# Optimization experiments

Measured on AMD Instinct MI355X. Metric: run time of the kernel, lower is better.

The kernel has to match this reference:

```python
import jax, jax.numpy as jnp
import numpy as np

N = 8192      # num nodes = feature dim (A is NxN adjacency used as features)
H = 1024      # bottleneck dim
E = 8192      # num edges
PENALTY = 10.0  # scalar buffer from __init__


def setup_inputs() -> dict:
    key = jax.random.key(0)
    ks = jax.random.split(key, 7)
    return {
        "A": jax.random.normal(ks[0], (N, N), dtype=jnp.float32),
        "W1": jax.random.normal(ks[1], (H, N), dtype=jnp.float32) * 0.02,
        "b1": jax.random.normal(ks[2], (H,), dtype=jnp.float32) * 0.02,
        "W2": jax.random.normal(ks[3], (N, H), dtype=jnp.float32) * 0.02,
        "b2": jax.random.normal(ks[4], (N,), dtype=jnp.float32) * 0.02,
        "edges": jax.random.randint(ks[5], (E, 2), 0, N, dtype=jnp.int32),
        "labels": jax.random.randint(ks[6], (E,), 0, 2, dtype=jnp.int32),
    }


def reference(A, W1, b1, W2, b2, edges, labels):
    ni = edges[:, 0]
    nj = edges[:, 1]
    Xi = A[ni]  # [E, N]
    Xj = A[nj]  # [E, N]
    lab = labels.astype(A.dtype)

    layers = [(W1, b1), (W2, b2)]
    Hi, Hj = Xi, Xj
    loss_1 = jnp.zeros((), A.dtype)
    loss_r_per_edge = jnp.zeros((), A.dtype)
    for (W, b) in layers:
        Hi = jax.nn.sigmoid(Hi @ W.T + b)
        Hj = jax.nn.sigmoid(Hj @ W.T + b)
        # per-edge L2 norm of activation diff at this layer, weighted by label
        loss_1 = loss_1 + jnp.sum(jnp.linalg.norm(Hi - Hj, axis=1) * lab)
        # original code appends weight-row-norm sum + bias norm once per (edge, layer)
        loss_r_per_edge = loss_r_per_edge + jnp.sum(jnp.linalg.norm(W, axis=1)) + jnp.linalg.norm(b)
    loss_r = loss_r_per_edge * jnp.asarray(E, A.dtype)

    # reconstruction loss; penalty scales the diff when label >= 1 (scalar => factors out of norm)
    factor = jnp.where(lab >= 1.0, jnp.asarray(PENALTY, A.dtype), jnp.asarray(1.0, A.dtype))
    loss_2 = jnp.sum(factor * (jnp.linalg.norm(Xi - Hi, axis=1) + jnp.linalg.norm(Xj - Hj, axis=1)))

    return loss_1 + loss_2 + loss_r
```

## Files before the change

### kernel.cpp

```cpp
#include <hip/hip_runtime.h>
#include <hip/hip_bf16.h>
#include <stdint.h>

#define N_DIM 8192
#define H_DIM 1024
#define E_DIM 8192
#define PENALTY_F 10.0f
#define WSCALE 16.0f
#define INV_WSCALE 0.0625f

typedef unsigned short u16;
typedef unsigned char u8;
typedef unsigned int u32;
typedef __attribute__((ext_vector_type(4))) float f32x4;
typedef __attribute__((ext_vector_type(2))) float f32x2;
typedef __attribute__((ext_vector_type(4))) int i32x4;
typedef __attribute__((ext_vector_type(8))) int i32x8;

__device__ __forceinline__ u32 pack4_fp8(float a, float b, float c, float d) {
  u32 p = __builtin_amdgcn_cvt_pk_fp8_f32(a, b, 0, false);
  p = __builtin_amdgcn_cvt_pk_fp8_f32(c, d, p, true);
  return p;
}
__device__ __forceinline__ f32x2 unpk_lo(u32 v) {
  return __builtin_amdgcn_cvt_pk_f32_fp8(v, false);
}
__device__ __forceinline__ f32x2 unpk_hi(u32 v) {
  return __builtin_amdgcn_cvt_pk_f32_fp8(v, true);
}

#define GLD16(ldsptr, gptr)                                                     \
  __builtin_amdgcn_global_load_lds(                                             \
      (__attribute__((address_space(1))) void*)(gptr),                          \
      (__attribute__((address_space(3))) void*)(ldsptr), 16, 0, 0)

#define PSLOT(part) (&(part)[(blockIdx.x & 63) * 16])

__device__ __forceinline__ float wave_red(float v) {
  for (int o = 32; o; o >>= 1) v += __shfl_down(v, o, 64);
  return v;
}

__device__ __forceinline__ float block_reduce1(float v) {
  __shared__ float buf[4];
  v = wave_red(v);
  int lane = threadIdx.x & 63, w = threadIdx.x >> 6;
  if (lane == 0) buf[w] = v;
  __syncthreads();
  float r = 0.f;
  if (threadIdx.x == 0) r = buf[0] + buf[1] + buf[2] + buf[3];
  return r;
}

__global__ void convert_f32_fp8(const float* __restrict__ in,
                                u8* __restrict__ out, int n4, float scale) {
  const int stride = gridDim.x * blockDim.x;
  for (int i = blockIdx.x * blockDim.x + threadIdx.x; i < n4; i += stride) {
    float4 v = ((const float4*)in)[i];
    ((u32*)out)[i] =
        pack4_fp8(v.x * scale, v.y * scale, v.z * scale, v.w * scale);
  }
}

__global__ void prep_w(const float* __restrict__ W1,
                       const float* __restrict__ W2,
                       const float* __restrict__ b1,
                       const float* __restrict__ b2, u8* __restrict__ W1_8,
                       u8* __restrict__ W2_8, float* __restrict__ part) {
  const int blk = blockIdx.x;
  float* slotp = PSLOT(part);
  if (blk < H_DIM) {
    const float4* row = (const float4*)(W1 + (size_t)blk * N_DIM);
    u32* orow = (u32*)(W1_8 + (size_t)blk * N_DIM);
    float s = 0.f;
#pragma unroll
    for (int t = 0; t < 8; ++t) {
      int i = threadIdx.x + t * 256;
      float4 v = row[i];
      s += v.x * v.x + v.y * v.y + v.z * v.z + v.w * v.w;
      orow[i] = pack4_fp8(v.x * WSCALE, v.y * WSCALE, v.z * WSCALE,
                          v.w * WSCALE);
    }
    s = block_reduce1(s);
    if (threadIdx.x == 0) atomicAdd(slotp, sqrtf(s) * (float)E_DIM);
  } else if (blk < H_DIM + N_DIM / 4) {
    __shared__ float buf[4];
    const int wave = threadIdx.x >> 6, lane = threadIdx.x & 63;
    const int r = (blk - H_DIM) * 4 + wave;
    const float4* row = (const float4*)(W2 + (size_t)r * H_DIM);
    u32* orow = (u32*)(W2_8 + (size_t)r * H_DIM);
    float s = 0.f;
#pragma unroll
    for (int t = 0; t < 4; ++t) {
      int i = lane + t * 64;
      float4 v = row[i];
      s += v.x * v.x + v.y * v.y + v.z * v.z + v.w * v.w;
      orow[i] = pack4_fp8(v.x * WSCALE, v.y * WSCALE, v.z * WSCALE,
                          v.w * WSCALE);
    }
    s = wave_red(s);
    if (lane == 0) buf[wave] = sqrtf(s);
    __syncthreads();
    if (threadIdx.x == 0)
      atomicAdd(slotp, (buf[0] + buf[1] + buf[2] + buf[3]) * (float)E_DIM);
  } else if (blk == H_DIM + N_DIM / 4) {
    const float4* row = (const float4*)b1;
    float4 v = row[threadIdx.x];
    float s = v.x * v.x + v.y * v.y + v.z * v.z + v.w * v.w;
    s = block_reduce1(s);
    if (threadIdx.x == 0) atomicAdd(slotp, sqrtf(s) * (float)E_DIM);
  } else {
    const float4* row = (const float4*)b2;
    float s = 0.f;
#pragma unroll
    for (int t = 0; t < 8; ++t) {
      float4 v = row[threadIdx.x + t * 256];
      s += v.x * v.x + v.y * v.y + v.z * v.z + v.w * v.w;
    }
    s = block_reduce1(s);
    if (threadIdx.x == 0) atomicAdd(slotp, sqrtf(s) * (float)E_DIM);
  }
}

#define BM 128
#define BN 128
#define BKB 128

__global__ __launch_bounds__(256) void gemm_fp8_sigmoid(
    const u8* __restrict__ Ag,
    const u8* __restrict__ Bg,
    const float* __restrict__ bias,
    u8* __restrict__ Cg,
    float invScale, int K, int Nd) {
  __shared__ __align__(16) u8 Xs[BM * BKB];
  __shared__ __align__(16) u8 Ws[BN * BKB];

  const int nwg = gridDim.x * gridDim.y;
  const int id = blockIdx.y * gridDim.x + blockIdx.x;
  const int wg = (id & 7) * (nwg >> 3) + (id >> 3);
  const int bx = wg % gridDim.x;
  const int by = wg / gridDim.x;

  const int tid = threadIdx.x;
  const int wave = tid >> 6, lane = tid & 63;
  const int wr = wave >> 1, wc = wave & 1;
  const size_t rowBase = (size_t)by * BM;
  const size_t colBase = (size_t)bx * BN;

  f32x4 acc[4][4] = {};

  const int i8 = lane >> 3;
  const int c8 = lane & 7;
  const int sw = c8 ^ i8;

  const int quad = lane >> 4;
  const int m15 = lane & 15;

  for (int k0 = 0; k0 < K; k0 += BKB) {
#pragma unroll
    for (int j = 0; j < 4; ++j) {
      const int r0 = (wave * 4 + j) * 8;
      const u8* gx = Ag + (rowBase + r0 + i8) * (size_t)K + (k0 + sw * 16);
      GLD16(&Xs[r0 * BKB], gx);
      const u8* gw = Bg + (colBase + r0 + i8) * (size_t)K + (k0 + sw * 16);
      GLD16(&Ws[r0 * BKB], gw);
    }
    __syncthreads();

    i32x8 af[4], bfr[4];
#pragma unroll
    for (int t = 0; t < 4; ++t) {
      const int m = wr * 64 + t * 16 + m15;
      i32x4 alo = *(const i32x4*)&Xs[m * BKB + ((2 * quad) ^ (m & 7)) * 16];
      i32x4 ahi = *(const i32x4*)&Xs[m * BKB + ((2 * quad + 1) ^ (m & 7)) * 16];
      af[t] = __builtin_shufflevector(alo, ahi, 0, 1, 2, 3, 4, 5, 6, 7);
      const int n = wc * 64 + t * 16 + m15;
      i32x4 blo = *(const i32x4*)&Ws[n * BKB + ((2 * quad) ^ (n & 7)) * 16];
      i32x4 bhi = *(const i32x4*)&Ws[n * BKB + ((2 * quad + 1) ^ (n & 7)) * 16];
      bfr[t] = __builtin_shufflevector(blo, bhi, 0, 1, 2, 3, 4, 5, 6, 7);
    }
#pragma unroll
    for (int mt = 0; mt < 4; ++mt)
#pragma unroll
      for (int nt = 0; nt < 4; ++nt)
        acc[mt][nt] = __builtin_amdgcn_mfma_scale_f32_16x16x128_f8f6f4(
            bfr[nt], af[mt], acc[mt][nt], 0, 0,
            0, 0x7F7F7F7F, 0, 0x7F7F7F7F);
    __syncthreads();
  }

  f32x4 bv4[4];
#pragma unroll
  for (int nt = 0; nt < 4; ++nt)
    bv4[nt] = *(const f32x4*)&bias[colBase + wc * 64 + nt * 16 + quad * 4];
#pragma unroll
  for (int mt = 0; mt < 4; ++mt) {
    const size_t grow = rowBase + wr * 64 + mt * 16 + m15;
    u32* crow = (u32*)(Cg + grow * (size_t)Nd + colBase + wc * 64);
#pragma unroll
    for (int nt = 0; nt < 4; ++nt) {
      float v[4];
#pragma unroll
      for (int i = 0; i < 4; ++i) {
        float x = acc[mt][nt][i] * invScale + bv4[nt][i];
        v[i] = WSCALE / (1.0f + __expf(-x));
      }
      crow[nt * 4 + quad] = pack4_fp8(v[0], v[1], v[2], v[3]);
    }
  }
}

#define BM2 256
#define BN2 256

__global__ __launch_bounds__(512, 2) void gemm2_fp8_sigmoid(
    const u8* __restrict__ Ag,
    const u8* __restrict__ Bg,
    const float* __restrict__ bias,
    u8* __restrict__ Cg,
    const u8* __restrict__ A8,
    float* __restrict__ nd2,
    float invScale, int K, int Nd) {
  __shared__ __align__(16) u8 Xs[2][BM2 * BKB];
  __shared__ __align__(16) u8 Ws[2][BN2 * BKB];

  const int tid = threadIdx.x;
  const int wave = tid >> 6, lane = tid & 63;
  const int wr = wave >> 2;
  const int wc = wave & 3;
  const size_t rowBase = (size_t)blockIdx.y * BM2;
  const size_t colBase = (size_t)blockIdx.x * BN2;

  f32x4 acc[8][4] = {};

  const int i8 = lane >> 3;
  const int c8 = lane & 7;
  const int sw = c8 ^ i8;
  const int quad = lane >> 4;
  const int m15 = lane & 15;

  const int T = K / BKB;

  auto STAGE = [&](int kt, int b) {
    const size_t kOff = (size_t)kt * BKB + sw * 16;
#pragma unroll
    for (int j = 0; j < 4; ++j) {
      const int r0 = (wave * 4 + j) * 8;
      GLD16(&Xs[b][r0 * BKB], Ag + (rowBase + r0 + i8) * (size_t)K + kOff);
      GLD16(&Ws[b][r0 * BKB], Bg + (colBase + r0 + i8) * (size_t)K + kOff);
    }
  };

  STAGE(0, 0);
  __syncthreads();

  for (int t = 0; t < T; ++t) {
    const int cur = t & 1;
    if (t + 1 < T) STAGE(t + 1, cur ^ 1);

    const u8* Xb = Xs[cur];
    const u8* Wb = Ws[cur];

    i32x8 bfr[4];
#pragma unroll
    for (int nt = 0; nt < 4; ++nt) {
      const int n = wc * 64 + nt * 16 + m15;
      i32x4 blo = *(const i32x4*)&Wb[n * BKB + ((2 * quad) ^ (n & 7)) * 16];
      i32x4 bhi = *(const i32x4*)&Wb[n * BKB + ((2 * quad + 1) ^ (n & 7)) * 16];
      bfr[nt] = __builtin_shufflevector(blo, bhi, 0, 1, 2, 3, 4, 5, 6, 7);
    }
    __builtin_amdgcn_s_setprio(1);
#pragma unroll
    for (int mt = 0; mt < 8; ++mt) {
      const int m = wr * 128 + mt * 16 + m15;
      i32x4 alo = *(const i32x4*)&Xb[m * BKB + ((2 * quad) ^ (m & 7)) * 16];
      i32x4 ahi = *(const i32x4*)&Xb[m * BKB + ((2 * quad + 1) ^ (m & 7)) * 16];
      i32x8 af = __builtin_shufflevector(alo, ahi, 0, 1, 2, 3, 4, 5, 6, 7);
#pragma unroll
      for (int nt = 0; nt < 4; ++nt)
        acc[mt][nt] = __builtin_amdgcn_mfma_scale_f32_16x16x128_f8f6f4(
            bfr[nt], af, acc[mt][nt], 0, 0,
            0, 0x7F7F7F7F, 0, 0x7F7F7F7F);
    }
    __builtin_amdgcn_s_setprio(0);
    __syncthreads();
  }

  float* ndbuf = (float*)&Xs[0][0];
  if (tid < 256) ndbuf[tid] = 0.f;
  __syncthreads();

  f32x4 bv4[4];
#pragma unroll
  for (int nt = 0; nt < 4; ++nt)
    bv4[nt] = *(const f32x4*)&bias[colBase + wc * 64 + nt * 16 + quad * 4];
#pragma unroll
  for (int mt = 0; mt < 8; ++mt) {
    const int rowLocal = wr * 128 + mt * 16 + m15;
    const size_t grow = rowBase + rowLocal;
    u32* crow = (u32*)(Cg + grow * (size_t)Nd + colBase + wc * 64);
    const u32* arow = (const u32*)(A8 + grow * (size_t)Nd + colBase + wc * 64);
    float nds = 0.f;
#pragma unroll
    for (int nt = 0; nt < 4; ++nt) {
      float v[4];
#pragma unroll
      for (int i = 0; i < 4; ++i) {
        float x = acc[mt][nt][i] * invScale + bv4[nt][i];
        v[i] = WSCALE / (1.0f + __expf(-x));
      }
      const u32 packed = pack4_fp8(v[0], v[1], v[2], v[3]);
      crow[nt * 4 + quad] = packed;
      f32x2 hlo = unpk_lo(packed), hhi = unpk_hi(packed);
      const u32 xa = arow[nt * 4 + quad];
      f32x2 xlo = unpk_lo(xa), xhi = unpk_hi(xa);
      float d;
      d = WSCALE * xlo.x - hlo.x; nds += d * d;
      d = WSCALE * xlo.y - hlo.y; nds += d * d;
      d = WSCALE * xhi.x - hhi.x; nds += d * d;
      d = WSCALE * xhi.y - hhi.y; nds += d * d;
    }
    atomicAdd(&ndbuf[rowLocal], nds);
  }
  __syncthreads();
  if (tid < 256) atomicAdd(&nd2[rowBase + tid], ndbuf[tid]);
}

__global__ void edge_loss_h(const u8* __restrict__ H1,
                            const int* __restrict__ edges,
                            const int* __restrict__ labels,
                            float* __restrict__ part) {
  __shared__ float buf[4];
  const int wave = threadIdx.x >> 6, lane = threadIdx.x & 63;
  const int e = blockIdx.x * 4 + wave;
  float r = 0.f;
  if (labels[e] != 0) {
    const int ni = edges[e * 2], nj = edges[e * 2 + 1];
    const i32x4 a = ((const i32x4*)(H1 + (size_t)ni * H_DIM))[lane];
    const i32x4 b = ((const i32x4*)(H1 + (size_t)nj * H_DIM))[lane];
    float s = 0.f;
#pragma unroll
    for (int j = 0; j < 4; ++j) {
      f32x2 al = unpk_lo((u32)a[j]), ah = unpk_hi((u32)a[j]);
      f32x2 bl = unpk_lo((u32)b[j]), bh = unpk_hi((u32)b[j]);
      float d0 = al.x - bl.x, d1 = al.y - bl.y;
      float d2 = ah.x - bh.x, d3 = ah.y - bh.y;
      s += d0 * d0 + d1 * d1 + d2 * d2 + d3 * d3;
    }
    s = wave_red(s);
    r = sqrtf(s) * INV_WSCALE;
  }
  if (lane == 0) buf[wave] = r;
  __syncthreads();
  if (threadIdx.x == 0)
    atomicAdd(PSLOT(part), buf[0] + buf[1] + buf[2] + buf[3]);
}

__global__ void edge_loss_final(const u8* __restrict__ H2,
                                const float* __restrict__ nd2,
                                const int* __restrict__ edges,
                                const int* __restrict__ labels,
                                float* __restrict__ part) {
  __shared__ float buf[4];
  const int wave = threadIdx.x >> 6, lane = threadIdx.x & 63;
  const int e = blockIdx.x * 4 + wave;
  const int ni = edges[e * 2], nj = edges[e * 2 + 1];
  const i32x4* hi = (const i32x4*)(H2 + (size_t)ni * N_DIM);
  const i32x4* hj = (const i32x4*)(H2 + (size_t)nj * N_DIM);
  float s12 = 0.f;
#pragma unroll 2
  for (int t = 0; t < 8; ++t) {
    const int idx = lane + t * 64;
    i32x4 a = hi[idx], b = hj[idx];
#pragma unroll
    for (int j = 0; j < 4; ++j) {
      f32x2 al = unpk_lo((u32)a[j]), ah = unpk_hi((u32)a[j]);
      f32x2 bl = unpk_lo((u32)b[j]), bh = unpk_hi((u32)b[j]);
      float d;
      d = al.x - bl.x; s12 += d * d;
      d = al.y - bl.y; s12 += d * d;
      d = ah.x - bh.x; s12 += d * d;
      d = ah.y - bh.y; s12 += d * d;
    }
  }
  s12 = wave_red(s12);
  if (lane == 0) {
    float lab = (labels[e] != 0) ? 1.f : 0.f;
    float fac = (labels[e] != 0) ? PENALTY_F : 1.f;
    buf[wave] = (lab * sqrtf(s12) + fac * (sqrtf(nd2[ni]) + sqrtf(nd2[nj]))) *
                INV_WSCALE;
  }
  __syncthreads();
  if (threadIdx.x == 0)
    atomicAdd(PSLOT(part), buf[0] + buf[1] + buf[2] + buf[3]);
}

__global__ void finalize_sum(const float* __restrict__ part,
                             float* __restrict__ out) {
  float v = part[threadIdx.x * 16];
  v = wave_red(v);
  if (threadIdx.x == 0) atomicAdd(out, v);
}

extern "C" void kernel_launch(void* const* d_in, const int* in_sizes, int n_in,
                              void* d_out, int out_size, void* d_ws,
                              size_t ws_size, hipStream_t stream) {
  const float* A = (const float*)d_in[0];
  const float* W1 = (const float*)d_in[1];
  const float* b1 = (const float*)d_in[2];
  const float* W2 = (const float*)d_in[3];
  const float* b2 = (const float*)d_in[4];
  const int* edges = (const int*)d_in[5];
  const int* labels = (const int*)d_in[6];
  float* out = (float*)d_out;

  char* ws = (char*)d_ws;
  u8* A8   = (u8*)(ws);
  u8* H1_8 = (u8*)(ws + 67108864ull);
  u8* H2_8 = (u8*)(ws + 75497472ull);
  u8* W1_8 = (u8*)(ws + 142606336ull);
  u8* W2_8 = (u8*)(ws + 150994944ull);
  float* nd2  = (float*)(ws + 159383552ull);
  float* part = (float*)(ws + 159416320ull);

  hipMemsetAsync(out, 0, sizeof(float), stream);
  hipMemsetAsync(nd2, 0, N_DIM * sizeof(float) + 64 * 16 * sizeof(float),
                 stream);

  convert_f32_fp8<<<2048, 256, 0, stream>>>(A, A8, N_DIM * N_DIM / 4, 1.0f);

  prep_w<<<H_DIM + N_DIM / 4 + 2, 256, 0, stream>>>(W1, W2, b1, b2, W1_8,
                                                    W2_8, part);

  gemm_fp8_sigmoid<<<dim3(H_DIM / BN, N_DIM / BM), 256, 0, stream>>>(
      A8, W1_8, b1, H1_8, INV_WSCALE, N_DIM, H_DIM);
  edge_loss_h<<<E_DIM / 4, 256, 0, stream>>>(H1_8, edges, labels, part);

  gemm2_fp8_sigmoid<<<dim3(N_DIM / BN2, N_DIM / BM2), 512, 0, stream>>>(
      H1_8, W2_8, b2, H2_8, A8, nd2, INV_WSCALE * INV_WSCALE, H_DIM, N_DIM);
  edge_loss_final<<<E_DIM / 4, 256, 0, stream>>>(H2_8, nd2, edges, labels,
                                                 part);

  finalize_sum<<<1, 64, 0, stream>>>(part, out);
}
```

Before: 653.8 us.

## Fuse prep and edge kernels, drop memsets, use per-block partial slots

The A fp8 conversion, the weight prep and the nd2 zeroing are merged into one launch, which removes both memsets. The two edge-loss kernels become one that reads H2 rows only for labelled edges, since unlabelled edges contribute nothing from that term. Global atomics into 64 hashed slots are replaced by deterministic per-block partial writes that a 256-thread finalize sums. gemm2 also pre-reduces the row-norm partials with shuffles before its LDS atomics. Together these cut launch overhead, atomic contention and edge-phase memory traffic, at the cost of a larger finalize reduction.

```diff
diff --git a/kernel.cpp b/kernel.cpp
--- a/kernel.cpp
+++ b/kernel.cpp
@@ -8,6 +8,9 @@
 #define PENALTY_F 10.0f
 #define WSCALE 16.0f
 #define INV_WSCALE 0.0625f
+
+#define PREP_SLOTS 3074
+#define EDGE_BASE 4096
 
 typedef unsigned short u16;
 typedef unsigned char u8;
@@ -33,8 +36,6 @@
   __builtin_amdgcn_global_load_lds(                                             \
       (__attribute__((address_space(1))) void*)(gptr),                          \
       (__attribute__((address_space(3))) void*)(ldsptr), 16, 0, 0)
-
-#define PSLOT(part) (&(part)[(blockIdx.x & 63) * 16])
 
 __device__ __forceinline__ float wave_red(float v) {
   for (int o = 32; o; o >>= 1) v += __shfl_down(v, o, 64);
@@ -52,23 +53,14 @@
   return r;
 }
 
-__global__ void convert_f32_fp8(const float* __restrict__ in,
-                                u8* __restrict__ out, int n4, float scale) {
-  const int stride = gridDim.x * blockDim.x;
-  for (int i = blockIdx.x * blockDim.x + threadIdx.x; i < n4; i += stride) {
-    float4 v = ((const float4*)in)[i];
-    ((u32*)out)[i] =
-        pack4_fp8(v.x * scale, v.y * scale, v.z * scale, v.w * scale);
-  }
-}
-
-__global__ void prep_w(const float* __restrict__ W1,
-                       const float* __restrict__ W2,
-                       const float* __restrict__ b1,
-                       const float* __restrict__ b2, u8* __restrict__ W1_8,
-                       u8* __restrict__ W2_8, float* __restrict__ part) {
+__global__ void prep_all(const float* __restrict__ A,
+                         const float* __restrict__ W1,
+                         const float* __restrict__ W2,
+                         const float* __restrict__ b1,
+                         const float* __restrict__ b2, u8* __restrict__ A8,
+                         u8* __restrict__ W1_8, u8* __restrict__ W2_8,
+                         float* __restrict__ nd2, float* __restrict__ part) {
   const int blk = blockIdx.x;
-  float* slotp = PSLOT(part);
   if (blk < H_DIM) {
     const float4* row = (const float4*)(W1 + (size_t)blk * N_DIM);
     u32* orow = (u32*)(W1_8 + (size_t)blk * N_DIM);
@@ -82,7 +74,7 @@
                           v.w * WSCALE);
     }
     s = block_reduce1(s);
-    if (threadIdx.x == 0) atomicAdd(slotp, sqrtf(s) * (float)E_DIM);
+    if (threadIdx.x == 0) part[blk] = sqrtf(s) * (float)E_DIM;
   } else if (blk < H_DIM + N_DIM / 4) {
     __shared__ float buf[4];
     const int wave = threadIdx.x >> 6, lane = threadIdx.x & 63;
@@ -102,14 +94,14 @@
     if (lane == 0) buf[wave] = sqrtf(s);
     __syncthreads();
     if (threadIdx.x == 0)
-      atomicAdd(slotp, (buf[0] + buf[1] + buf[2] + buf[3]) * (float)E_DIM);
+      part[blk] = (buf[0] + buf[1] + buf[2] + buf[3]) * (float)E_DIM;
   } else if (blk == H_DIM + N_DIM / 4) {
     const float4* row = (const float4*)b1;
     float4 v = row[threadIdx.x];
     float s = v.x * v.x + v.y * v.y + v.z * v.z + v.w * v.w;
     s = block_reduce1(s);
-    if (threadIdx.x == 0) atomicAdd(slotp, sqrtf(s) * (float)E_DIM);
-  } else {
+    if (threadIdx.x == 0) part[blk] = sqrtf(s) * (float)E_DIM;
+  } else if (blk == H_DIM + N_DIM / 4 + 1) {
     const float4* row = (const float4*)b2;
     float s = 0.f;
 #pragma unroll
@@ -118,7 +110,19 @@
       s += v.x * v.x + v.y * v.y + v.z * v.z + v.w * v.w;
     }
     s = block_reduce1(s);
-    if (threadIdx.x == 0) atomicAdd(slotp, sqrtf(s) * (float)E_DIM);
+    if (threadIdx.x == 0) part[blk] = sqrtf(s) * (float)E_DIM;
+  } else if (blk == PREP_SLOTS) {
+    f32x4 z = {0.f, 0.f, 0.f, 0.f};
+#pragma unroll
+    for (int t = 0; t < 8; ++t)
+      ((f32x4*)nd2)[threadIdx.x + t * 256] = z;
+  } else {
+    const int cb = blk - (PREP_SLOTS + 1);
+    const int n4 = N_DIM * N_DIM / 4;
+    for (int i = cb * 256 + threadIdx.x; i < n4; i += 2048 * 256) {
+      float4 v = ((const float4*)A)[i];
+      ((u32*)A8)[i] = pack4_fp8(v.x, v.y, v.z, v.w);
+    }
   }
 }
 
@@ -320,86 +324,79 @@
       d = WSCALE * xhi.x - hhi.x; nds += d * d;
       d = WSCALE * xhi.y - hhi.y; nds += d * d;
     }
-    atomicAdd(&ndbuf[rowLocal], nds);
+    nds += __shfl_down(nds, 32, 64);
+    nds += __shfl_down(nds, 16, 64);
+    if (lane < 16) atomicAdd(&ndbuf[rowLocal], nds);
   }
   __syncthreads();
   if (tid < 256) atomicAdd(&nd2[rowBase + tid], ndbuf[tid]);
 }
 
-__global__ void edge_loss_h(const u8* __restrict__ H1,
-                            const int* __restrict__ edges,
-                            const int* __restrict__ labels,
-                            float* __restrict__ part) {
-  __shared__ float buf[4];
-  const int wave = threadIdx.x >> 6, lane = threadIdx.x & 63;
-  const int e = blockIdx.x * 4 + wave;
-  float r = 0.f;
-  if (labels[e] != 0) {
-    const int ni = edges[e * 2], nj = edges[e * 2 + 1];
-    const i32x4 a = ((const i32x4*)(H1 + (size_t)ni * H_DIM))[lane];
-    const i32x4 b = ((const i32x4*)(H1 + (size_t)nj * H_DIM))[lane];
-    float s = 0.f;
-#pragma unroll
-    for (int j = 0; j < 4; ++j) {
-      f32x2 al = unpk_lo((u32)a[j]), ah = unpk_hi((u32)a[j]);
-      f32x2 bl = unpk_lo((u32)b[j]), bh = unpk_hi((u32)b[j]);
-      float d0 = al.x - bl.x, d1 = al.y - bl.y;
-      float d2 = ah.x - bh.x, d3 = ah.y - bh.y;
-      s += d0 * d0 + d1 * d1 + d2 * d2 + d3 * d3;
-    }
-    s = wave_red(s);
-    r = sqrtf(s) * INV_WSCALE;
-  }
-  if (lane == 0) buf[wave] = r;
-  __syncthreads();
-  if (threadIdx.x == 0)
-    atomicAdd(PSLOT(part), buf[0] + buf[1] + buf[2] + buf[3]);
-}
-
-__global__ void edge_loss_final(const u8* __restrict__ H2,
-                                const float* __restrict__ nd2,
-                                const int* __restrict__ edges,
-                                const int* __restrict__ labels,
-                                float* __restrict__ part) {
+__global__ void edge_all(const u8* __restrict__ H1, const u8* __restrict__ H2,
+                         const float* __restrict__ nd2,
+                         const int* __restrict__ edges,
+                         const int* __restrict__ labels,
+                         float* __restrict__ part) {
   __shared__ float buf[4];
   const int wave = threadIdx.x >> 6, lane = threadIdx.x & 63;
   const int e = blockIdx.x * 4 + wave;
   const int ni = edges[e * 2], nj = edges[e * 2 + 1];
-  const i32x4* hi = (const i32x4*)(H2 + (size_t)ni * N_DIM);
-  const i32x4* hj = (const i32x4*)(H2 + (size_t)nj * N_DIM);
-  float s12 = 0.f;
+  const int lab = labels[e];
+  float r = 0.f;
+  if (lab != 0) {
+    const i32x4 a1 = ((const i32x4*)(H1 + (size_t)ni * H_DIM))[lane];
+    const i32x4 b1v = ((const i32x4*)(H1 + (size_t)nj * H_DIM))[lane];
+    float s1 = 0.f;
+#pragma unroll
+    for (int j = 0; j < 4; ++j) {
+      f32x2 al = unpk_lo((u32)a1[j]), ah = unpk_hi((u32)a1[j]);
+      f32x2 bl = unpk_lo((u32)b1v[j]), bh = unpk_hi((u32)b1v[j]);
+      float d0 = al.x - bl.x, d1 = al.y - bl.y;
+      float d2 = ah.x - bh.x, d3 = ah.y - bh.y;
+      s1 += d0 * d0 + d1 * d1 + d2 * d2 + d3 * d3;
+    }
+    const i32x4* hi = (const i32x4*)(H2 + (size_t)ni * N_DIM);
+    const i32x4* hj = (const i32x4*)(H2 + (size_t)nj * N_DIM);
+    float s12 = 0.f;
 #pragma unroll 2
-  for (int t = 0; t < 8; ++t) {
-    const int idx = lane + t * 64;
-    i32x4 a = hi[idx], b = hj[idx];
-#pragma unroll
-    for (int j = 0; j < 4; ++j) {
-      f32x2 al = unpk_lo((u32)a[j]), ah = unpk_hi((u32)a[j]);
-      f32x2 bl = unpk_lo((u32)b[j]), bh = unpk_hi((u32)b[j]);
-      float d;
-      d = al.x - bl.x; s12 += d * d;
-      d = al.y - bl.y; s12 += d * d;
-      d = ah.x - bh.x; s12 += d * d;
-      d = ah.y - bh.y; s12 += d * d;
-    }
-  }
-  s12 = wave_red(s12);
+    for (int t = 0; t < 8; ++t) {
+      const int idx = lane + t * 64;
+      i32x4 a = hi[idx], b = hj[idx];
+#pragma unroll
+      for (int j = 0; j < 4; ++j) {
+        f32x2 al = unpk_lo((u32)a[j]), ah = unpk_hi((u32)a[j]);
+        f32x2 bl = unpk_lo((u32)b[j]), bh = unpk_hi((u32)b[j]);
+        float d;
+        d = al.x - bl.x; s12 += d * d;
+        d = al.y - bl.y; s12 += d * d;
+        d = ah.x - bh.x; s12 += d * d;
+        d = ah.y - bh.y; s12 += d * d;
+      }
+    }
+    for (int o = 32; o; o >>= 1) {
+      s1 += __shfl_down(s1, o, 64);
+      s12 += __shfl_down(s12, o, 64);
+    }
+    r = (sqrtf(s1) + sqrtf(s12)) * INV_WSCALE;
+  }
   if (lane == 0) {
-    float lab = (labels[e] != 0) ? 1.f : 0.f;
-    float fac = (labels[e] != 0) ? PENALTY_F : 1.f;
-    buf[wave] = (lab * sqrtf(s12) + fac * (sqrtf(nd2[ni]) + sqrtf(nd2[nj]))) *
-                INV_WSCALE;
+    const float fac = (lab != 0) ? PENALTY_F : 1.f;
+    r += fac * (sqrtf(nd2[ni]) + sqrtf(nd2[nj])) * INV_WSCALE;
+    buf[wave] = r;
   }
   __syncthreads();
   if (threadIdx.x == 0)
-    atomicAdd(PSLOT(part), buf[0] + buf[1] + buf[2] + buf[3]);
+    part[EDGE_BASE + blockIdx.x] = buf[0] + buf[1] + buf[2] + buf[3];
 }
 
 __global__ void finalize_sum(const float* __restrict__ part,
                              float* __restrict__ out) {
-  float v = part[threadIdx.x * 16];
-  v = wave_red(v);
-  if (threadIdx.x == 0) atomicAdd(out, v);
+  float s = 0.f;
+  for (int i = threadIdx.x; i < PREP_SLOTS; i += 256) s += part[i];
+  for (int i = EDGE_BASE + threadIdx.x; i < EDGE_BASE + E_DIM / 4; i += 256)
+    s += part[i];
+  s = block_reduce1(s);
+  if (threadIdx.x == 0) *out = s;
 }
 
 extern "C" void kernel_launch(void* const* d_in, const int* in_sizes, int n_in,
@@ -423,23 +420,17 @@
   float* nd2  = (float*)(ws + 159383552ull);
   float* part = (float*)(ws + 159416320ull);
 
-  hipMemsetAsync(out, 0, sizeof(float), stream);
-  hipMemsetAsync(nd2, 0, N_DIM * sizeof(float) + 64 * 16 * sizeof(float),
-                 stream);
-
-  convert_f32_fp8<<<2048, 256, 0, stream>>>(A, A8, N_DIM * N_DIM / 4, 1.0f);
-
-  prep_w<<<H_DIM + N_DIM / 4 + 2, 256, 0, stream>>>(W1, W2, b1, b2, W1_8,
-                                                    W2_8, part);
+  prep_all<<<PREP_SLOTS + 1 + 2048, 256, 0, stream>>>(A, W1, W2, b1, b2, A8,
+                                                      W1_8, W2_8, nd2, part);
 
   gemm_fp8_sigmoid<<<dim3(H_DIM / BN, N_DIM / BM), 256, 0, stream>>>(
       A8, W1_8, b1, H1_8, INV_WSCALE, N_DIM, H_DIM);
-  edge_loss_h<<<E_DIM / 4, 256, 0, stream>>>(H1_8, edges, labels, part);
 
   gemm2_fp8_sigmoid<<<dim3(N_DIM / BN2, N_DIM / BM2), 512, 0, stream>>>(
       H1_8, W2_8, b2, H2_8, A8, nd2, INV_WSCALE * INV_WSCALE, H_DIM, N_DIM);
-  edge_loss_final<<<E_DIM / 4, 256, 0, stream>>>(H2_8, nd2, edges, labels,
-                                                 part);
-
-  finalize_sum<<<1, 64, 0, stream>>>(part, out);
-}
+
+  edge_all<<<E_DIM / 4, 256, 0, stream>>>(H1_8, H2_8, nd2, edges, labels,
+                                          part);
+
+  finalize_sum<<<1, 256, 0, stream>>>(part, out);
+}
```

Result: no change. 651.5 us (-0.3%).
